# Performance work log

Measured on AMD Instinct MI355X. Metric: run time of the kernel, lower is better.

## Reference

```python
import jax, jax.numpy as jnp
import numpy as np

# pywt db4 decomposition filters (dec_lo, dec_hi), 8 taps
DEC_LO = np.array([-0.010597401784997278, 0.032883011666982945, 0.030841381835986965,
                   -0.18703481171888114, -0.02798376941698385, 0.6308807679295904,
                   0.7148465705525415, 0.23037781330885523])
DEC_HI = np.array([-0.23037781330885523, 0.7148465705525415, -0.6308807679295904,
                   -0.02798376941698385, 0.18703481171888114, 0.030841381835986965,
                   -0.032883011666982945, -0.010597401784997278])
HEADS = 8


def dwt_db4(v):
    # Equivalent of pywt.dwt(v, 'db4') (mode='symmetric') applied along last axis.
    # Symmetric (half-point) extension by L-1=7, full convolution, downsample taking
    # every 2nd sample starting at conv index 1 -> out_len = floor((n+7)/2).
    pad = [(0, 0)] * (v.ndim - 1) + [(7, 7)]
    ext = jnp.pad(v, pad, mode='symmetric')[..., 1:]
    lead = v.shape[:-1]
    lhs = ext.reshape(-1, 1, ext.shape[-1])                       # (N, 1, n+13)
    rhs = jnp.stack([jnp.asarray(DEC_LO[::-1], v.dtype),
                     jnp.asarray(DEC_HI[::-1], v.dtype)])[:, None, :]  # (2, 1, 8)
    out = jax.lax.conv_general_dilated(lhs, rhs, (2,), 'VALID')   # (N, 2, out_len)
    out = out.reshape(*lead, 2, -1)
    return out[..., 0, :], out[..., 1, :]


def setup_inputs() -> dict:
    key = jax.random.key(0)
    k0, k1, k2, k3 = jax.random.split(key, 4)
    B, S, H = 4, 2048, 1024
    a = float(np.sqrt(6.0 / (H + H)))  # xavier_uniform bound
    x = jax.random.normal(k0, (B, S, H), dtype=jnp.float32)
    Wq = jax.random.uniform(k1, (H, H), jnp.float32, -a, a)
    Wk = jax.random.uniform(k2, (H, H), jnp.float32, -a, a)
    Wv = jax.random.uniform(k3, (H, H), jnp.float32, -a, a)
    return {"x": x, "Wq": Wq, "Wk": Wk, "Wv": Wv}


def reference(x, Wq, Wk, Wv):
    B, S, Hd = x.shape
    H = HEADS
    dk = Hd // H
    scale = dk ** -0.5
    # torch nn.Linear: y = x @ W.T
    q = (x @ Wq.T).reshape(B, S, H, dk).transpose(0, 2, 1, 3) * scale  # (B,H,S,dk)
    k = (x @ Wk.T).reshape(B, S, H, dk).transpose(0, 2, 1, 3)
    v = (x @ Wv.T).reshape(B, S, H, dk).transpose(0, 2, 1, 3)
    attn = jax.nn.softmax(jnp.einsum('bhqd,bhkd->bhqk', q, k), axis=-1)
    cA, cD = dwt_db4(v)                                   # (B,H,S,wA) each
    wA = cA.shape[-1]
    wcD = jnp.einsum('bhqk,bhkw->bhqw', attn, cD)
    out1 = wcD.transpose(0, 2, 1, 3).reshape(B, S, H * wA)
    out2 = cA.reshape(-1, S, H * wA)                      # faithful raw view of (B,H,S,wA)
    return out1, out2
```

## Files before the change

### kernel.cpp

```cpp
#include <hip/hip_runtime.h>
#include <hip/hip_bf16.h>

#define B_ 4
#define S_ 2048
#define HD 1024
#define NH 8
#define DK 128
#define WA 67
#define WPAD 80

typedef __attribute__((ext_vector_type(8))) short short8;
typedef __attribute__((ext_vector_type(4))) short short4v;
typedef __attribute__((ext_vector_type(4))) float floatx4;

__device__ __forceinline__ float hexp2(float x) { return __builtin_amdgcn_exp2f(x); }

__device__ __forceinline__ short f2bf(float f) {
    union { float f; unsigned u; } c; c.f = f;
    unsigned u = c.u;
    u += 0x7FFF + ((u >> 16) & 1);
    return (short)(u >> 16);
}
__device__ __forceinline__ float bf2f(short s) {
    union { unsigned u; float f; } c; c.u = ((unsigned)(unsigned short)s) << 16;
    return c.f;
}
__device__ __forceinline__ short f2bf_trunc(float f) {
    union { float f; unsigned u; } c; c.f = f;
    return (short)(c.u >> 16);
}

__device__ __forceinline__ void glds16(void* lds, const void* g) {
    __builtin_amdgcn_global_load_lds(
        (const __attribute__((address_space(1))) unsigned*)g,
        (__attribute__((address_space(3))) unsigned*)lds, 16, 0, 0);
}

__device__ __constant__ float FLO[8] = {
    0.23037781330885523f,  0.7148465705525415f,  0.6308807679295904f,
   -0.02798376941698385f, -0.18703481171888114f, 0.030841381835986965f,
    0.032883011666982945f, -0.010597401784997278f };
__device__ __constant__ float FHI[8] = {
   -0.010597401784997278f, -0.032883011666982945f, 0.030841381835986965f,
    0.18703481171888114f,  -0.02798376941698385f, -0.6308807679295904f,
    0.7148465705525415f,   -0.23037781330885523f };

__global__ __launch_bounds__(256) void cvt_all(
    const float* __restrict__ x,  const float* __restrict__ wq,
    const float* __restrict__ wk, const float* __restrict__ wv,
    short* __restrict__ xb, short* __restrict__ wb)
{
    const size_t w_elems = (size_t)HD * HD;
    int blk = blockIdx.x;
    const float* src; short* dst; int lb;
    if (blk < 4096)      { src = x;  dst = xb;               lb = blk; }
    else if (blk < 4608) { src = wq; dst = wb;               lb = blk - 4096; }
    else if (blk < 5120) { src = wk; dst = wb + w_elems;     lb = blk - 4608; }
    else                 { src = wv; dst = wb + 2 * w_elems; lb = blk - 5120; }
    int i = lb * 256 + threadIdx.x;
    const float4* s = (const float4*)src + (size_t)i * 2;
    float4 f0 = s[0], f1 = s[1];
    short8 o;
    o[0] = f2bf(f0.x); o[1] = f2bf(f0.y); o[2] = f2bf(f0.z); o[3] = f2bf(f0.w);
    o[4] = f2bf(f1.x); o[5] = f2bf(f1.y); o[6] = f2bf(f1.z); o[7] = f2bf(f1.w);
    *((short8*)dst + i) = o;
}

__global__ __launch_bounds__(256) void qkv_gemm(
    const short* __restrict__ xb, const short* __restrict__ Wb,
    short* __restrict__ Qb, short* __restrict__ Kb,
    float* __restrict__ outA, short* __restrict__ cdt)
{
    __shared__ __align__(16) short smem[128 * 134];
    short* As = smem;
    short* Bs = smem + 128 * 64;
    short* Cs = smem;
    const int tid  = threadIdx.x;
    const int wv   = tid >> 6;
    const int lane = tid & 63;
    const int l15  = lane & 15;
    const int quad = lane >> 4;
    const int m0 = blockIdx.x * 128;
    const int n0 = blockIdx.y * 128;
    const int z  = blockIdx.z;
    const short* W = Wb + (size_t)z * HD * HD;
    const float scale = (z == 0) ? 0.12751743786072596f : 1.0f;
    const int wm = (wv & 1) * 64;
    const int wn = (wv >> 1) * 64;
    const int srow = lane >> 3;
    const int sch  = (lane & 7) ^ (srow & 7);
    const int rxor = (l15 & 7);

    floatx4 acc[4][4] = {};
    for (int kk = 0; kk < HD; kk += 64) {
        __syncthreads();
        #pragma unroll
        for (int i = 0; i < 4; ++i) {
            int ti = wv * 4 + i;
            int r  = ti * 8 + srow;
            glds16(As + ti * 512, xb + (size_t)(m0 + r) * HD + kk + sch * 8);
            glds16(Bs + ti * 512, W  + (size_t)(n0 + r) * HD + kk + sch * 8);
        }
        __syncthreads();
        #pragma unroll
        for (int s4 = 0; s4 < 2; ++s4) {
            short8 a[4], b[4];
            #pragma unroll
            for (int t = 0; t < 4; ++t) {
                int ch = (s4 * 4 + quad) ^ rxor;
                a[t] = *(const short8*)&As[(wm + t * 16 + l15) * 64 + ch * 8];
                b[t] = *(const short8*)&Bs[(wn + t * 16 + l15) * 64 + ch * 8];
            }
            #pragma unroll
            for (int mt = 0; mt < 4; ++mt)
                #pragma unroll
                for (int nt = 0; nt < 4; ++nt)
                    acc[mt][nt] = __builtin_amdgcn_mfma_f32_16x16x32_bf16(
                        a[mt], b[nt], acc[mt][nt], 0, 0, 0);
        }
    }
    if (z != 2) {
        short* Yb = (z == 0) ? Qb : Kb;
        #pragma unroll
        for (int mt = 0; mt < 4; ++mt)
            #pragma unroll
            for (int nt = 0; nt < 4; ++nt)
                #pragma unroll
                for (int reg = 0; reg < 4; ++reg) {
                    int rg = m0 + wm + mt * 16 + quad * 4 + reg;
                    int cg = n0 + wn + nt * 16 + l15;
                    int b = rg >> 11, s = rg & 2047;
                    int h = cg >> 7,  d = cg & 127;
                    Yb[((size_t)(b * NH + h) * S_ + s) * DK + d] =
                        f2bf(acc[mt][nt][reg] * scale);
                }
        return;
    }
    __syncthreads();
    #pragma unroll
    for (int mt = 0; mt < 4; ++mt)
        #pragma unroll
        for (int nt = 0; nt < 4; ++nt)
            #pragma unroll
            for (int reg = 0; reg < 4; ++reg)
                Cs[(wm + mt * 16 + quad * 4 + reg) * 134 + wn + nt * 16 + l15] =
                    f2bf(acc[mt][nt][reg]);
    __syncthreads();
    const int rl    = tid & 127;
    const int chunk = tid >> 7;
    const int rg = m0 + rl;
    const int b = rg >> 11, s = rg & 2047;
    const int bh = b * NH + blockIdx.y;
    const short* vr = Cs + rl * 134;
    auto getv = [&](int i) -> float {
        int k = (i < 6) ? (5 - i) : (i < 134) ? (i - 6) : (261 - i);
        return bf2f(vr[k]);
    };
    const int t0 = chunk * 34;
    const int t1 = (chunk == 0) ? 34 : WA;
    float win[8];
    #pragma unroll
    for (int j = 0; j < 8; ++j) win[j] = getv(2 * t0 + j);
    float* oA = outA + ((size_t)bh * S_ + s) * WA;
    for (int t = t0; t < t1; ++t) {
        float lo = 0.f, hi = 0.f;
        #pragma unroll
        for (int j = 0; j < 8; ++j) { lo += win[j] * FLO[j]; hi += win[j] * FHI[j]; }
        oA[t] = lo;
        cdt[((size_t)bh * WPAD + t) * S_ + s] = f2bf(hi);
        #pragma unroll
        for (int j = 0; j < 6; ++j) win[j] = win[j + 2];
        if (t + 1 < t1) { win[6] = getv(2 * t + 8); win[7] = getv(2 * t + 9); }
    }
    if (chunk == 1) {
        #pragma unroll
        for (int w = WA; w < WPAD; ++w)
            cdt[((size_t)bh * WPAD + w) * S_ + s] =
                (w == 67) ? (short)0x3F80 : (short)0;
    }
}

__global__ __launch_bounds__(256, 2) void attn_kernel(
    const short* __restrict__ Qb, const short* __restrict__ Kb,
    const short* __restrict__ cdt, float* __restrict__ out1)
{
    __shared__ __align__(16) short Ks[64 * 128];
    __shared__ __align__(16) short Ds[WPAD * 64];
    __shared__ __align__(16) short Pt[8 * 1024];
    const int tid  = threadIdx.x;
    const int wv   = tid >> 6;
    const int lane = tid & 63;
    const int l15  = lane & 15;
    const int quad = lane >> 4;
    const int qt = blockIdx.x;
    const int bh = blockIdx.y;
    const int b = bh >> 3, h = bh & 7;
    const int rxor = l15 & 7;

    short8 aq[2][4];
    #pragma unroll
    for (int n = 0; n < 2; ++n) {
        const short* qrow =
            Qb + ((size_t)bh * S_ + qt * 128 + wv * 32 + n * 16 + l15) * DK;
        #pragma unroll
        for (int s4 = 0; s4 < 4; ++s4)
            aq[n][s4] = *(const short8*)(qrow + s4 * 32 + quad * 8);
    }

    floatx4 O[2][5] = {};

    const short* kbase = Kb + (size_t)bh * S_ * DK;
    const int krow = lane >> 4;
    const int kch  = (lane & 15);
    const int drow = lane >> 3;
    const int dch  = (lane & 7) ^ (drow & 7);
    short* ptw = Pt + wv * 2048;

    for (int kt = 0; kt < 32; ++kt) {
        __syncthreads();
        #pragma unroll
        for (int i = 0; i < 4; ++i) {
            int ti = wv * 4 + i;
            int r  = ti * 4 + krow;
            int ch = kch ^ (r & 7);
            glds16(Ks + ti * 512, kbase + ((size_t)kt * 64 + r) * DK + ch * 8);
        }
        #pragma unroll
        for (int i = 0; i < 3; ++i) {
            int t = wv + i * 4;
            if (t < 10) {
                int r = t * 8 + drow;
                glds16(Ds + t * 512,
                       cdt + ((size_t)bh * WPAD + r) * S_ + kt * 64 + dch * 8);
            }
        }
        __syncthreads();

        floatx4 sc[2][4] = {};
        #pragma unroll
        for (int s4 = 0; s4 < 4; ++s4) {
            short8 kf[4];
            #pragma unroll
            for (int mt = 0; mt < 4; ++mt) {
                int ch = (s4 * 4 + quad) ^ rxor;
                kf[mt] = *(const short8*)&Ks[(mt * 16 + l15) * 128 + ch * 8];
            }
            #pragma unroll
            for (int n = 0; n < 2; ++n)
                #pragma unroll
                for (int mt = 0; mt < 4; ++mt)
                    sc[n][mt] = __builtin_amdgcn_mfma_f32_16x16x32_bf16(
                        kf[mt], aq[n][s4], sc[n][mt], 0, 0, 0);
        }
        #pragma unroll
        for (int n = 0; n < 2; ++n) {
            #pragma unroll
            for (int mt = 0; mt < 4; ++mt) {
                short4v pk;
                #pragma unroll
                for (int reg = 0; reg < 4; ++reg)
                    pk[reg] = f2bf_trunc(hexp2(sc[n][mt][reg]));
                int ch = (mt * 2 + (quad >> 1)) ^ rxor;
                *(short4v*)&ptw[n * 1024 + l15 * 64 + ch * 8 + (quad & 1) * 4] = pk;
            }
        }
        short8 ap[2][2];
        #pragma unroll
        for (int mt = 0; mt < 2; ++mt)
            #pragma unroll
            for (int ks = 0; ks < 2; ++ks) {
                int ch = (ks * 4 + quad) ^ rxor;
                ap[mt][ks] = *(const short8*)&ptw[mt * 1024 + l15 * 64 + ch * 8];
            }
        #pragma unroll
        for (int j = 0; j < 5; ++j) {
            #pragma unroll
            for (int ks = 0; ks < 2; ++ks) {
                int ch = (ks * 4 + quad) ^ rxor;
                short8 bd = *(const short8*)&Ds[(j * 16 + l15) * 64 + ch * 8];
                #pragma unroll
                for (int mt = 0; mt < 2; ++mt)
                    O[mt][j] = __builtin_amdgcn_mfma_f32_16x16x32_bf16(
                        ap[mt][ks], bd, O[mt][j], 0, 0, 0);
            }
        }
    }
    float rl[2][4];
    #pragma unroll
    for (int mt = 0; mt < 2; ++mt)
        #pragma unroll
        for (int reg = 0; reg < 4; ++reg)
            rl[mt][reg] = 1.0f / __shfl(O[mt][4][reg], (quad << 4) | 3, 64);
    #pragma unroll
    for (int mt = 0; mt < 2; ++mt)
        #pragma unroll
        for (int j = 0; j < 5; ++j) {
            int w = j * 16 + l15;
            if (w < WA) {
                #pragma unroll
                for (int reg = 0; reg < 4; ++reg) {
                    int qrow_g = qt * 128 + wv * 32 + mt * 16 + quad * 4 + reg;
                    out1[((size_t)(b * S_ + qrow_g)) * (NH * WA) + h * WA + w] =
                        O[mt][j][reg] * rl[mt][reg];
                }
            }
        }
}

extern "C" void kernel_launch(void* const* d_in, const int* in_sizes, int n_in,
                              void* d_out, int out_size, void* d_ws, size_t ws_size,
                              hipStream_t stream)
{
    const float* x  = (const float*)d_in[0];
    const float* Wq = (const float*)d_in[1];
    const float* Wk = (const float*)d_in[2];
    const float* Wv = (const float*)d_in[3];
    float* out = (float*)d_out;

    const size_t x_elems   = (size_t)B_ * S_ * HD;
    const size_t w_elems   = (size_t)HD * HD;
    const size_t qkv_elems = (size_t)B_ * NH * S_ * DK;
    short* xb  = (short*)d_ws;
    short* Wb  = xb + x_elems;
    short* Qb  = Wb + 3 * w_elems;
    short* Kb  = Qb + qkv_elems;
    short* cdt = Kb + qkv_elems;
    float* out1 = out;
    float* out2 = out + (size_t)B_ * S_ * NH * WA;

    cvt_all<<<dim3(5632), 256, 0, stream>>>(x, Wq, Wk, Wv, xb, Wb);
    qkv_gemm<<<dim3(64, 8, 3), 256, 0, stream>>>(xb, Wb, Qb, Kb, out2, cdt);
    attn_kernel<<<dim3(16, 32), 256, 0, stream>>>(Qb, Kb, cdt, out1);
}
```

Before: 230.6 us.

## Rewrite QKV GEMM as 256x256 tile, 8-wave, double-buffered pipelined kernel

The QKV projection GEMM moves from 128x128 tiles with 4 waves and a single LDS buffer to 256x256 tiles with 8 waves, split into four 128x128 quadrant phases over a double-buffered LDS ring. Global-to-LDS loads for upcoming k-steps are issued between phases and guarded by manual vmcnt waits and raw barriers, and MFMA sections run at raised wave priority. The aim is to hide load latency behind compute and to raise operand reuse per byte loaded. The cost is 128KB of LDS per block, which limits occupancy, plus fragile hand-tuned waitcnt sync. The DWT epilogue is adapted to handle two heads per block.

Result: slower. 242.0 us (+5.0%).

```diff
diff --git a/kernel.cpp b/kernel.cpp
--- a/kernel.cpp
+++ b/kernel.cpp
@@ -66,118 +66,177 @@
     *((short8*)dst + i) = o;
 }
 
-__global__ __launch_bounds__(256) void qkv_gemm(
+__global__ __launch_bounds__(512, 2) void qkv_gemm(
     const short* __restrict__ xb, const short* __restrict__ Wb,
     short* __restrict__ Qb, short* __restrict__ Kb,
     float* __restrict__ outA, short* __restrict__ cdt)
 {
-    __shared__ __align__(16) short smem[128 * 134];
-    short* As = smem;
-    short* Bs = smem + 128 * 64;
-    short* Cs = smem;
+    __shared__ __align__(16) short lds[2][2][2][8192];
     const int tid  = threadIdx.x;
-    const int wv   = tid >> 6;
+    const int wid  = tid >> 6;
     const int lane = tid & 63;
     const int l15  = lane & 15;
     const int quad = lane >> 4;
-    const int m0 = blockIdx.x * 128;
-    const int n0 = blockIdx.y * 128;
-    const int z  = blockIdx.z;
+    const int rxor = l15 & 7;
+    const int wm   = wid >> 2;
+    const int wq   = wid & 3;
+    const int m0 = blockIdx.x * 256;
+    const int by = blockIdx.y;
+    const int z  = by >> 2;
+    const int nz0 = (by & 3) * 256;
     const short* W = Wb + (size_t)z * HD * HD;
     const float scale = (z == 0) ? 0.12751743786072596f : 1.0f;
-    const int wm = (wv & 1) * 64;
-    const int wn = (wv >> 1) * 64;
-    const int srow = lane >> 3;
-    const int sch  = (lane & 7) ^ (srow & 7);
-    const int rxor = (l15 & 7);
-
-    floatx4 acc[4][4] = {};
-    for (int kk = 0; kk < HD; kk += 64) {
-        __syncthreads();
-        #pragma unroll
-        for (int i = 0; i < 4; ++i) {
-            int ti = wv * 4 + i;
-            int r  = ti * 8 + srow;
-            glds16(As + ti * 512, xb + (size_t)(m0 + r) * HD + kk + sch * 8);
-            glds16(Bs + ti * 512, W  + (size_t)(n0 + r) * HD + kk + sch * 8);
-        }
-        __syncthreads();
-        #pragma unroll
-        for (int s4 = 0; s4 < 2; ++s4) {
-            short8 a[4], b[4];
-            #pragma unroll
-            for (int t = 0; t < 4; ++t) {
-                int ch = (s4 * 4 + quad) ^ rxor;
-                a[t] = *(const short8*)&As[(wm + t * 16 + l15) * 64 + ch * 8];
-                b[t] = *(const short8*)&Bs[(wn + t * 16 + l15) * 64 + ch * 8];
-            }
-            #pragma unroll
-            for (int mt = 0; mt < 4; ++mt)
-                #pragma unroll
-                for (int nt = 0; nt < 4; ++nt)
-                    acc[mt][nt] = __builtin_amdgcn_mfma_f32_16x16x32_bf16(
-                        a[mt], b[nt], acc[mt][nt], 0, 0, 0);
-        }
-    }
+
+    floatx4 acc[2][2][4][2] = {};
+
+    auto stA = [&](int bf, int hf, int t) {
+        const short* g = xb + (size_t)(m0 + hf * 128) * HD + t * 64;
+        short* slot = &lds[bf][0][hf][0];
+        #pragma unroll
+        for (int i = 0; i < 2; ++i) {
+            int ti = wid * 2 + i;
+            int r  = ti * 8 + (lane >> 3);
+            int ch = (lane & 7) ^ (lane >> 3);
+            glds16(slot + ti * 512, g + (size_t)r * HD + ch * 8);
+        }
+    };
+    auto stB = [&](int bf, int hf, int t) {
+        const short* g = W + (size_t)(nz0 + hf * 128) * HD + t * 64;
+        short* slot = &lds[bf][1][hf][0];
+        #pragma unroll
+        for (int i = 0; i < 2; ++i) {
+            int ti = wid * 2 + i;
+            int r  = ti * 8 + (lane >> 3);
+            int ch = (lane & 7) ^ (lane >> 3);
+            glds16(slot + ti * 512, g + (size_t)r * HD + ch * 8);
+        }
+    };
+
+#define VM8 asm volatile("s_waitcnt vmcnt(8)" ::: "memory")
+#define BARRIER do { asm volatile("" ::: "memory"); \
+                     __builtin_amdgcn_s_barrier(); \
+                     asm volatile("" ::: "memory"); } while (0)
+#define PHASE(MH, NH, STG) do { \
+    short8 afr[4][2], bfr[2][2]; \
+    const short* Ab = &lds[cur][0][MH][0]; \
+    const short* Bb = &lds[cur][1][NH][0]; \
+    _Pragma("unroll") \
+    for (int mt = 0; mt < 4; ++mt) { \
+        const int rr = (wm * 64 + mt * 16 + l15) * 64; \
+        afr[mt][0] = *(const short8*)&Ab[rr + ((quad ^ rxor) * 8)]; \
+        afr[mt][1] = *(const short8*)&Ab[rr + (((4 + quad) ^ rxor) * 8)]; \
+    } \
+    _Pragma("unroll") \
+    for (int nt = 0; nt < 2; ++nt) { \
+        const int rr = (wq * 32 + nt * 16 + l15) * 64; \
+        bfr[nt][0] = *(const short8*)&Bb[rr + ((quad ^ rxor) * 8)]; \
+        bfr[nt][1] = *(const short8*)&Bb[rr + (((4 + quad) ^ rxor) * 8)]; \
+    } \
+    STG; \
+    BARRIER; \
+    __builtin_amdgcn_s_setprio(1); \
+    _Pragma("unroll") \
+    for (int ks = 0; ks < 2; ++ks) \
+        _Pragma("unroll") \
+        for (int mt = 0; mt < 4; ++mt) \
+            _Pragma("unroll") \
+            for (int nt = 0; nt < 2; ++nt) \
+                acc[MH][NH][mt][nt] = __builtin_amdgcn_mfma_f32_16x16x32_bf16( \
+                    afr[mt][ks], bfr[nt][ks], acc[MH][NH][mt][nt], 0, 0, 0); \
+    __builtin_amdgcn_s_setprio(0); \
+} while (0)
+
+    stB(0, 0, 0); stA(0, 0, 0); stA(0, 1, 0); stB(0, 1, 0);
+    stB(1, 0, 1); stA(1, 0, 1);
+    VM8; BARRIER;
+
+    #pragma unroll 2
+    for (int t = 0; t < 16; ++t) {
+        const int cur = t & 1, nxt = cur ^ 1;
+        const int ta = (t + 1) & 15, tb = (t + 2) & 15;
+        PHASE(0, 0, stA(nxt, 1, ta)); VM8; BARRIER;
+        PHASE(1, 0, stB(nxt, 1, ta)); VM8; BARRIER;
+        PHASE(0, 1, stB(cur, 0, tb));      BARRIER;
+        PHASE(1, 1, stA(cur, 0, tb)); VM8; BARRIER;
+    }
+    __syncthreads();
+
     if (z != 2) {
         short* Yb = (z == 0) ? Qb : Kb;
         #pragma unroll
-        for (int mt = 0; mt < 4; ++mt)
-            #pragma unroll
-            for (int nt = 0; nt < 4; ++nt)
-                #pragma unroll
-                for (int reg = 0; reg < 4; ++reg) {
-                    int rg = m0 + wm + mt * 16 + quad * 4 + reg;
-                    int cg = n0 + wn + nt * 16 + l15;
-                    int b = rg >> 11, s = rg & 2047;
-                    int h = cg >> 7,  d = cg & 127;
-                    Yb[((size_t)(b * NH + h) * S_ + s) * DK + d] =
-                        f2bf(acc[mt][nt][reg] * scale);
-                }
+        for (int mh = 0; mh < 2; ++mh)
+            #pragma unroll
+            for (int nh = 0; nh < 2; ++nh)
+                #pragma unroll
+                for (int mt = 0; mt < 4; ++mt)
+                    #pragma unroll
+                    for (int nt = 0; nt < 2; ++nt)
+                        #pragma unroll
+                        for (int reg = 0; reg < 4; ++reg) {
+                            int rg = m0 + mh * 128 + wm * 64 + mt * 16 + quad * 4 + reg;
+                            int cg = nz0 + nh * 128 + wq * 32 + nt * 16 + l15;
+                            int b = rg >> 11, s = rg & 2047;
+                            int h = cg >> 7,  d = cg & 127;
+                            Yb[((size_t)(b * NH + h) * S_ + s) * DK + d] =
+                                f2bf(acc[mh][nh][mt][nt][reg] * scale);
+                        }
         return;
     }
-    __syncthreads();
+    short* Cs = &lds[0][0][0][0];
+    const int rl    = tid & 127;
+    const int hl    = (tid >> 7) & 1;
+    const int chunk = tid >> 8;
     #pragma unroll
-    for (int mt = 0; mt < 4; ++mt)
-        #pragma unroll
-        for (int nt = 0; nt < 4; ++nt)
-            #pragma unroll
-            for (int reg = 0; reg < 4; ++reg)
-                Cs[(wm + mt * 16 + quad * 4 + reg) * 134 + wn + nt * 16 + l15] =
-                    f2bf(acc[mt][nt][reg]);
-    __syncthreads();
-    const int rl    = tid & 127;
-    const int chunk = tid >> 7;
-    const int rg = m0 + rl;
-    const int b = rg >> 11, s = rg & 2047;
-    const int bh = b * NH + blockIdx.y;
-    const short* vr = Cs + rl * 134;
-    auto getv = [&](int i) -> float {
-        int k = (i < 6) ? (5 - i) : (i < 134) ? (i - 6) : (261 - i);
-        return bf2f(vr[k]);
-    };
-    const int t0 = chunk * 34;
-    const int t1 = (chunk == 0) ? 34 : WA;
-    float win[8];
-    #pragma unroll
-    for (int j = 0; j < 8; ++j) win[j] = getv(2 * t0 + j);
-    float* oA = outA + ((size_t)bh * S_ + s) * WA;
-    for (int t = t0; t < t1; ++t) {
-        float lo = 0.f, hi = 0.f;
-        #pragma unroll
-        for (int j = 0; j < 8; ++j) { lo += win[j] * FLO[j]; hi += win[j] * FHI[j]; }
-        oA[t] = lo;
-        cdt[((size_t)bh * WPAD + t) * S_ + s] = f2bf(hi);
-        #pragma unroll
-        for (int j = 0; j < 6; ++j) win[j] = win[j + 2];
-        if (t + 1 < t1) { win[6] = getv(2 * t + 8); win[7] = getv(2 * t + 9); }
-    }
-    if (chunk == 1) {
-        #pragma unroll
-        for (int w = WA; w < WPAD; ++w)
-            cdt[((size_t)bh * WPAD + w) * S_ + s] =
-                (w == 67) ? (short)0x3F80 : (short)0;
-    }
+    for (int mh = 0; mh < 2; ++mh) {
+        __syncthreads();
+        #pragma unroll
+        for (int nh = 0; nh < 2; ++nh)
+            #pragma unroll
+            for (int mt = 0; mt < 4; ++mt)
+                #pragma unroll
+                for (int nt = 0; nt < 2; ++nt)
+                    #pragma unroll
+                    for (int reg = 0; reg < 4; ++reg) {
+                        int r = wm * 64 + mt * 16 + quad * 4 + reg;
+                        int c = nh * 128 + wq * 32 + nt * 16 + l15;
+                        Cs[r * 258 + c] = f2bf(acc[mh][nh][mt][nt][reg]);
+                    }
+        __syncthreads();
+        const int rg = m0 + mh * 128 + rl;
+        const int b = rg >> 11, s = rg & 2047;
+        const int hg = (by & 3) * 2 + hl;
+        const int bh = b * NH + hg;
+        const short* vr = Cs + rl * 258 + hl * 128;
+        auto getv = [&](int i) -> float {
+            int k = (i < 6) ? (5 - i) : (i < 134) ? (i - 6) : (261 - i);
+            return bf2f(vr[k]);
+        };
+        const int t0  = chunk * 34;
+        const int t1c = (chunk == 0) ? 34 : WA;
+        float win[8];
+        #pragma unroll
+        for (int j = 0; j < 8; ++j) win[j] = getv(2 * t0 + j);
+        float* oA = outA + ((size_t)bh * S_ + s) * WA;
+        for (int t = t0; t < t1c; ++t) {
+            float lo = 0.f, hi = 0.f;
+            #pragma unroll
+            for (int j = 0; j < 8; ++j) { lo += win[j] * FLO[j]; hi += win[j] * FHI[j]; }
+            oA[t] = lo;
+            cdt[((size_t)bh * WPAD + t) * S_ + s] = f2bf(hi);
+            #pragma unroll
+            for (int j = 0; j < 6; ++j) win[j] = win[j + 2];
+            if (t + 1 < t1c) { win[6] = getv(2 * t + 8); win[7] = getv(2 * t + 9); }
+        }
+        if (chunk == 1) {
+            #pragma unroll
+            for (int w = WA; w < WPAD; ++w)
+                cdt[((size_t)bh * WPAD + w) * S_ + s] =
+                    (w == 67) ? (short)0x3F80 : (short)0;
+        }
+    }
+#undef PHASE
+#undef BARRIER
+#undef VM8
 }
 
 __global__ __launch_bounds__(256, 2) void attn_kernel(
@@ -329,6 +388,6 @@
     float* out2 = out + (size_t)B_ * S_ * NH * WA;
 
     cvt_all<<<dim3(5632), 256, 0, stream>>>(x, Wq, Wk, Wv, xb, Wb);
-    qkv_gemm<<<dim3(64, 8, 3), 256, 0, stream>>>(xb, Wb, Qb, Kb, out2, cdt);
+    qkv_gemm<<<dim3(32, 12), 512, 0, stream>>>(xb, Wb, Qb, Kb, out2, cdt);
     attn_kernel<<<dim3(16, 32), 256, 0, stream>>>(Qb, Kb, cdt, out1);
 }
```

## Triple-buffer QKV GEMM with 256x128 tiles, 8 waves and async prefetch

Applied to the files above, without the earlier changes.

Rewrites the QKV projection GEMM to use 512-thread blocks over 256x128 output tiles. The K-loop is software-pipelined with a three-stage LDS ring and the global-to-LDS loads are issued two steps ahead. Fine-grained vmcnt waits and raw barriers replace the two full syncthreads per step, and s_setprio raises priority around the MFMA bursts. The aim is to hide global load latency and raise MFMA utilization, at the cost of more LDS per block (about 144 KB), which limits occupancy to one block per CU. The DWT epilogue now handles 256 rows with a 130-short pitch.

Result: no change. 233.8 us (+1.4%).

```diff
diff --git a/kernel.cpp b/kernel.cpp
--- a/kernel.cpp
+++ b/kernel.cpp
@@ -66,59 +66,111 @@
     *((short8*)dst + i) = o;
 }
 
-__global__ __launch_bounds__(256) void qkv_gemm(
+__global__ __launch_bounds__(512) void qkv_gemm(
     const short* __restrict__ xb, const short* __restrict__ Wb,
     short* __restrict__ Qb, short* __restrict__ Kb,
     float* __restrict__ outA, short* __restrict__ cdt)
 {
-    __shared__ __align__(16) short smem[128 * 134];
-    short* As = smem;
-    short* Bs = smem + 128 * 64;
-    short* Cs = smem;
+    __shared__ __align__(16) short Asb[3][256 * 64];
+    __shared__ __align__(16) short Bsb[3][128 * 64];
     const int tid  = threadIdx.x;
-    const int wv   = tid >> 6;
+    const int wid  = tid >> 6;
     const int lane = tid & 63;
     const int l15  = lane & 15;
     const int quad = lane >> 4;
-    const int m0 = blockIdx.x * 128;
-    const int n0 = blockIdx.y * 128;
-    const int z  = blockIdx.z;
+    const int rx   = l15 & 7;
+    const int wm   = wid >> 1;
+    const int wn   = wid & 1;
+    const int m0 = blockIdx.x * 256;
+    const int by = blockIdx.y;
+    const int z  = by >> 3;
+    const int n0 = (by & 7) * 128;
     const short* W = Wb + (size_t)z * HD * HD;
     const float scale = (z == 0) ? 0.12751743786072596f : 1.0f;
-    const int wm = (wv & 1) * 64;
-    const int wn = (wv >> 1) * 64;
     const int srow = lane >> 3;
-    const int sch  = (lane & 7) ^ (srow & 7);
-    const int rxor = (l15 & 7);
+    const int sch  = (lane & 7) ^ srow;
 
     floatx4 acc[4][4] = {};
-    for (int kk = 0; kk < HD; kk += 64) {
-        __syncthreads();
+
+    auto stA = [&](int bf, int t) {
         #pragma unroll
         for (int i = 0; i < 4; ++i) {
-            int ti = wv * 4 + i;
-            int r  = ti * 8 + srow;
-            glds16(As + ti * 512, xb + (size_t)(m0 + r) * HD + kk + sch * 8);
-            glds16(Bs + ti * 512, W  + (size_t)(n0 + r) * HD + kk + sch * 8);
-        }
-        __syncthreads();
-        #pragma unroll
-        for (int s4 = 0; s4 < 2; ++s4) {
-            short8 a[4], b[4];
-            #pragma unroll
-            for (int t = 0; t < 4; ++t) {
-                int ch = (s4 * 4 + quad) ^ rxor;
-                a[t] = *(const short8*)&As[(wm + t * 16 + l15) * 64 + ch * 8];
-                b[t] = *(const short8*)&Bs[(wn + t * 16 + l15) * 64 + ch * 8];
-            }
+            int ti = wid * 4 + i;
+            glds16(&Asb[bf][ti * 512],
+                   xb + (size_t)(m0 + ti * 8 + srow) * HD + t * 64 + sch * 8);
+        }
+    };
+    auto stB = [&](int bf, int t) {
+        #pragma unroll
+        for (int i = 0; i < 2; ++i) {
+            int ti = wid * 2 + i;
+            glds16(&Bsb[bf][ti * 512],
+                   W + (size_t)(n0 + ti * 8 + srow) * HD + t * 64 + sch * 8);
+        }
+    };
+
+#define VM6 asm volatile("s_waitcnt vmcnt(6)" ::: "memory")
+#define VM0 asm volatile("s_waitcnt vmcnt(0)" ::: "memory")
+#define BARRIER do { asm volatile("" ::: "memory"); \
+                     __builtin_amdgcn_s_barrier(); \
+                     asm volatile("" ::: "memory"); } while (0)
+
+    stA(0, 0); stB(0, 0);
+    stA(1, 1); stB(1, 1);
+    VM6; BARRIER;
+
+    #pragma unroll
+    for (int t = 0; t < 16; ++t) {
+        const int cur = t % 3;
+        const int sb  = (t + 2) % 3;
+        {
+            short8 af[4], bf4[4];
+            #pragma unroll
+            for (int mt = 0; mt < 4; ++mt)
+                af[mt] = *(const short8*)
+                    &Asb[cur][(wm * 64 + mt * 16 + l15) * 64 + ((quad ^ rx) * 8)];
+            #pragma unroll
+            for (int nt = 0; nt < 4; ++nt)
+                bf4[nt] = *(const short8*)
+                    &Bsb[cur][(wn * 64 + nt * 16 + l15) * 64 + ((quad ^ rx) * 8)];
+            if (t < 14) stA(sb, t + 2);
+            BARRIER;
+            __builtin_amdgcn_s_setprio(1);
             #pragma unroll
             for (int mt = 0; mt < 4; ++mt)
                 #pragma unroll
                 for (int nt = 0; nt < 4; ++nt)
                     acc[mt][nt] = __builtin_amdgcn_mfma_f32_16x16x32_bf16(
-                        a[mt], b[nt], acc[mt][nt], 0, 0, 0);
-        }
-    }
+                        af[mt], bf4[nt], acc[mt][nt], 0, 0, 0);
+            __builtin_amdgcn_s_setprio(0);
+            BARRIER;
+        }
+        {
+            short8 af[4], bf4[4];
+            #pragma unroll
+            for (int mt = 0; mt < 4; ++mt)
+                af[mt] = *(const short8*)
+                    &Asb[cur][(wm * 64 + mt * 16 + l15) * 64 + (((4 + quad) ^ rx) * 8)];
+            #pragma unroll
+            for (int nt = 0; nt < 4; ++nt)
+                bf4[nt] = *(const short8*)
+                    &Bsb[cur][(wn * 64 + nt * 16 + l15) * 64 + (((4 + quad) ^ rx) * 8)];
+            if (t < 14) stB(sb, t + 2);
+            if (t < 14) { VM6; } else if (t == 14) { VM0; }
+            BARRIER;
+            __builtin_amdgcn_s_setprio(1);
+            #pragma unroll
+            for (int mt = 0; mt < 4; ++mt)
+                #pragma unroll
+                for (int nt = 0; nt < 4; ++nt)
+                    acc[mt][nt] = __builtin_amdgcn_mfma_f32_16x16x32_bf16(
+                        af[mt], bf4[nt], acc[mt][nt], 0, 0, 0);
+            __builtin_amdgcn_s_setprio(0);
+            BARRIER;
+        }
+    }
+    __syncthreads();
+
     if (z != 2) {
         short* Yb = (z == 0) ? Qb : Kb;
         #pragma unroll
@@ -127,8 +179,8 @@
             for (int nt = 0; nt < 4; ++nt)
                 #pragma unroll
                 for (int reg = 0; reg < 4; ++reg) {
-                    int rg = m0 + wm + mt * 16 + quad * 4 + reg;
-                    int cg = n0 + wn + nt * 16 + l15;
+                    int rg = m0 + wm * 64 + mt * 16 + quad * 4 + reg;
+                    int cg = n0 + wn * 64 + nt * 16 + l15;
                     int b = rg >> 11, s = rg & 2047;
                     int h = cg >> 7,  d = cg & 127;
                     Yb[((size_t)(b * NH + h) * S_ + s) * DK + d] =
@@ -136,22 +188,24 @@
                 }
         return;
     }
+    short* Cs = &Asb[0][0];
+    #pragma unroll
+    for (int mt = 0; mt < 4; ++mt)
+        #pragma unroll
+        for (int nt = 0; nt < 4; ++nt)
+            #pragma unroll
+            for (int reg = 0; reg < 4; ++reg) {
+                int r = wm * 64 + mt * 16 + quad * 4 + reg;
+                int c = wn * 64 + nt * 16 + l15;
+                Cs[r * 130 + c] = f2bf(acc[mt][nt][reg]);
+            }
     __syncthreads();
-    #pragma unroll
-    for (int mt = 0; mt < 4; ++mt)
-        #pragma unroll
-        for (int nt = 0; nt < 4; ++nt)
-            #pragma unroll
-            for (int reg = 0; reg < 4; ++reg)
-                Cs[(wm + mt * 16 + quad * 4 + reg) * 134 + wn + nt * 16 + l15] =
-                    f2bf(acc[mt][nt][reg]);
-    __syncthreads();
-    const int rl    = tid & 127;
-    const int chunk = tid >> 7;
+    const int rl    = tid & 255;
+    const int chunk = tid >> 8;
     const int rg = m0 + rl;
     const int b = rg >> 11, s = rg & 2047;
-    const int bh = b * NH + blockIdx.y;
-    const short* vr = Cs + rl * 134;
+    const int bh = b * NH + (by & 7);
+    const short* vr = Cs + rl * 130;
     auto getv = [&](int i) -> float {
         int k = (i < 6) ? (5 - i) : (i < 134) ? (i - 6) : (261 - i);
         return bf2f(vr[k]);
@@ -178,6 +232,9 @@
             cdt[((size_t)bh * WPAD + w) * S_ + s] =
                 (w == 67) ? (short)0x3F80 : (short)0;
     }
+#undef BARRIER
+#undef VM6
+#undef VM0
 }
 
 __global__ __launch_bounds__(256, 2) void attn_kernel(
@@ -329,6 +386,6 @@
     float* out2 = out + (size_t)B_ * S_ * NH * WA;
 
     cvt_all<<<dim3(5632), 256, 0, stream>>>(x, Wq, Wk, Wv, xb, Wb);
-    qkv_gemm<<<dim3(64, 8, 3), 256, 0, stream>>>(xb, Wb, Qb, Kb, out2, cdt);
+    qkv_gemm<<<dim3(32, 24), 512, 0, stream>>>(xb, Wb, Qb, Kb, out2, cdt);
     attn_kernel<<<dim3(16, 32), 256, 0, stream>>>(Qb, Kb, cdt, out1);
 }
```
